# Kernel optimization log

Measured on AMD Instinct MI355X. Metric: run time of the kernel, lower is better.

The kernel has to match this reference:

```python
import jax, jax.numpy as jnp
import numpy as np

DIM = 1024
NUM_HEADS = 16
NUM_KV_HEADS = 4
HEAD_DIM = DIM // NUM_HEADS
ROPE_BASE = 10000.0
EPS = 1e-8
BSZ, SEQ = 8, 1024


def setup_inputs() -> dict:
    key = jax.random.key(0)
    ks = jax.random.split(key, 6)
    x = jax.random.normal(ks[0], (BSZ, SEQ, DIM), dtype=jnp.float32)
    Wq = jax.random.normal(ks[1], (DIM, DIM), dtype=jnp.float32) * 0.02
    Wk = jax.random.normal(ks[2], (NUM_KV_HEADS * HEAD_DIM, DIM), dtype=jnp.float32) * 0.02
    Wv = jax.random.normal(ks[3], (NUM_KV_HEADS * HEAD_DIM, DIM), dtype=jnp.float32) * 0.02
    Wp = jax.random.normal(ks[4], (DIM, DIM), dtype=jnp.float32) * 0.02
    q_gain = jnp.ones((NUM_HEADS,), dtype=jnp.float32)  # qk_gain_init = 1.0
    return {"x": x, "Wq": Wq, "Wk": Wk, "Wv": Wv, "Wp": Wp, "q_gain": q_gain}


def bitlinear(x, w, eps=EPS):
    # weight ternarization (no-grad scale) with STE
    alpha = jax.lax.stop_gradient(jnp.maximum(jnp.mean(jnp.abs(w)), eps))
    w_t = jnp.round(jnp.clip(w / alpha, -1.0, 1.0))
    w_q = w + jax.lax.stop_gradient(w_t * alpha - w)
    # per-token int8 activation fake-quant with STE
    gamma = jax.lax.stop_gradient(
        jnp.maximum(jnp.max(jnp.abs(x), axis=-1, keepdims=True), eps) / 127.0)
    x_int = jnp.round(jnp.clip(x / gamma, -128.0, 127.0))
    x_q = x + jax.lax.stop_gradient(x_int * gamma - x)
    return (x_q @ (w_q / alpha).T) * alpha


def rms_norm(x):
    eps = jnp.finfo(x.dtype).eps
    return x * jax.lax.rsqrt(jnp.mean(x * x, axis=-1, keepdims=True) + eps)


def rope_cache(seq_len, head_dim, base):
    inv_freq = 1.0 / base ** (jnp.arange(0, head_dim, 2, dtype=jnp.float32) / head_dim)
    t = jnp.arange(seq_len, dtype=jnp.float32)
    freqs = jnp.outer(t, inv_freq)  # [S, hd/2]
    return jnp.cos(freqs), jnp.sin(freqs)


def apply_rotary(x, cos, sin):
    # x: [B,H,S,D]; cos/sin: [S,D/2] broadcast over B,H
    half = x.shape[-1] // 2
    x1, x2 = x[..., :half], x[..., half:]
    return jnp.concatenate((x1 * cos + x2 * sin, -x1 * sin + x2 * cos), axis=-1)


def reference(x, Wq, Wk, Wv, Wp, q_gain):
    bsz, seqlen, dim = x.shape
    q = bitlinear(x, Wq).reshape(bsz, seqlen, NUM_HEADS, HEAD_DIM).transpose(0, 2, 1, 3)
    k = bitlinear(x, Wk).reshape(bsz, seqlen, NUM_KV_HEADS, HEAD_DIM).transpose(0, 2, 1, 3)
    v = bitlinear(x, Wv).reshape(bsz, seqlen, NUM_KV_HEADS, HEAD_DIM).transpose(0, 2, 1, 3)
    q = rms_norm(q)
    k = rms_norm(k)
    cos, sin = rope_cache(seqlen, HEAD_DIM, ROPE_BASE)
    q = apply_rotary(q, cos, sin)
    k = apply_rotary(k, cos, sin)
    q = q * q_gain[None, :, None, None]
    # GQA: repeat kv heads
    rep = NUM_HEADS // NUM_KV_HEADS
    k = jnp.repeat(k, rep, axis=1)
    v = jnp.repeat(v, rep, axis=1)
    scale = 1.0 / jnp.sqrt(jnp.float32(HEAD_DIM))
    scores = jnp.einsum('bhqd,bhkd->bhqk', q, k) * scale
    causal = jnp.tril(jnp.ones((seqlen, seqlen), dtype=bool))
    scores = jnp.where(causal, scores, jnp.finfo(scores.dtype).min)
    attn = jax.nn.softmax(scores, axis=-1)
    y = jnp.einsum('bhqk,bhkd->bhqd', attn, v)
    y = y.transpose(0, 2, 1, 3).reshape(bsz, seqlen, dim)
    return bitlinear(y, Wp)
```

## Files before the change

### kernel.cpp

```cpp
#include <hip/hip_runtime.h>
#include <cmath>

#define DIMM 1024
#define NHEADS 16
#define NKV 4
#define HD 64
#define SEQ 1024
#define BSZ 8
#define ROWS (BSZ * SEQ)

typedef unsigned short u16;
typedef signed char s8;
typedef __attribute__((ext_vector_type(8))) short bf16x8;
typedef __attribute__((ext_vector_type(4))) float f32x4;
typedef __attribute__((ext_vector_type(4))) int i32x4;
typedef __attribute__((ext_vector_type(4))) unsigned short u16x4;

static __device__ __forceinline__ u16 f2bf(float f) {
    union { float f; unsigned u; } v; v.f = f;
    unsigned r = v.u + 0x7FFFu + ((v.u >> 16) & 1u);
    return (u16)(r >> 16);
}
static __device__ __forceinline__ float bf2f(u16 h) {
    union { unsigned u; float f; } v; v.u = ((unsigned)h) << 16;
    return v.f;
}

static __device__ __forceinline__ void gload16(const void* g, void* l) {
    __builtin_amdgcn_global_load_lds(
        (const __attribute__((address_space(1))) unsigned int*)g,
        (__attribute__((address_space(3))) unsigned int*)l, 16, 0, 0);
}

__global__ __launch_bounds__(256) void k_absmean_all(const float* __restrict__ Wq,
                                                     const float* __restrict__ Wk,
                                                     const float* __restrict__ Wv,
                                                     const float* __restrict__ Wp,
                                                     float* __restrict__ partial) {
    int wi = blockIdx.x >> 6, local = blockIdx.x & 63;
    const float* w = (wi == 0) ? Wq : (wi == 1) ? Wk : (wi == 2) ? Wv : Wp;
    int n = (wi == 0 || wi == 3) ? 1048576 : 262144;
    float s = 0.f;
    for (int i = local * 256 + threadIdx.x; i < n; i += 64 * 256) s += fabsf(w[i]);
    #pragma unroll
    for (int off = 32; off; off >>= 1) s += __shfl_xor(s, off);
    __shared__ float red[4];
    if ((threadIdx.x & 63) == 0) red[threadIdx.x >> 6] = s;
    __syncthreads();
    if (threadIdx.x == 0) partial[blockIdx.x] = red[0] + red[1] + red[2] + red[3];
}

__global__ __launch_bounds__(256) void k_rope_alpha(float* __restrict__ c, float* __restrict__ s,
                                                    const float* __restrict__ partial,
                                                    float* __restrict__ alpha) {
    int idx = blockIdx.x * 256 + threadIdx.x;
    int t = idx >> 5, i = idx & 31;
    float inv = 1.0f / powf(10000.0f, (float)(2 * i) * (1.0f / 64.0f));
    float f = (float)t * inv;
    c[idx] = cosf(f);
    s[idx] = sinf(f);
    if (blockIdx.x == 0 && threadIdx.x < 4) {
        const int ns[4] = {1048576, 262144, 262144, 1048576};
        float su = 0.f;
        for (int j = 0; j < 64; ++j) su += partial[threadIdx.x * 64 + j];
        alpha[threadIdx.x] = fmaxf(su / (float)ns[threadIdx.x], 1e-8f);
    }
}

__global__ __launch_bounds__(256) void k_tern_all(const float* __restrict__ Wq,
                                                  const float* __restrict__ Wk,
                                                  const float* __restrict__ Wv,
                                                  const float* __restrict__ Wp,
                                                  const float* __restrict__ alpha,
                                                  s8* __restrict__ wtqkv,
                                                  s8* __restrict__ wtp) {
    int idx = blockIdx.x * 256 + threadIdx.x;
    const float* src; s8* dst; float a;
    if (idx < 262144)      { src = Wq + (size_t)idx * 4;            dst = wtqkv + (size_t)idx * 4;                 a = alpha[0]; }
    else if (idx < 327680) { src = Wk + (size_t)(idx - 262144) * 4; dst = wtqkv + 1048576 + (size_t)(idx - 262144) * 4; a = alpha[1]; }
    else if (idx < 393216) { src = Wv + (size_t)(idx - 327680) * 4; dst = wtqkv + 1310720 + (size_t)(idx - 327680) * 4; a = alpha[2]; }
    else                   { src = Wp + (size_t)(idx - 393216) * 4; dst = wtp + (size_t)(idx - 393216) * 4;        a = alpha[3]; }
    float4 v = *reinterpret_cast<const float4*>(src);
    int q0 = (int)rintf(fminf(fmaxf(v.x / a, -1.f), 1.f));
    int q1 = (int)rintf(fminf(fmaxf(v.y / a, -1.f), 1.f));
    int q2 = (int)rintf(fminf(fmaxf(v.z / a, -1.f), 1.f));
    int q3 = (int)rintf(fminf(fmaxf(v.w / a, -1.f), 1.f));
    *reinterpret_cast<unsigned*>(dst) =
        (q0 & 0xff) | ((q1 & 0xff) << 8) | ((q2 & 0xff) << 16) | ((q3 & 0xff) << 24);
}

__global__ __launch_bounds__(256) void k_quant(const float* __restrict__ X,
                                               s8* __restrict__ Xq, float* __restrict__ g) {
    int row = blockIdx.x;
    const float* xr = X + (size_t)row * DIMM;
    float4 v = *reinterpret_cast<const float4*>(&xr[threadIdx.x * 4]);
    float mv = fmaxf(fmaxf(fabsf(v.x), fabsf(v.y)), fmaxf(fabsf(v.z), fabsf(v.w)));
    #pragma unroll
    for (int off = 32; off; off >>= 1) mv = fmaxf(mv, __shfl_xor(mv, off));
    __shared__ float red[4];
    if ((threadIdx.x & 63) == 0) red[threadIdx.x >> 6] = mv;
    __syncthreads();
    mv = fmaxf(fmaxf(red[0], red[1]), fmaxf(red[2], red[3]));
    float gamma = fmaxf(mv, 1e-8f) / 127.0f;
    int q0 = (int)rintf(fminf(fmaxf(v.x / gamma, -128.f), 127.f));
    int q1 = (int)rintf(fminf(fmaxf(v.y / gamma, -128.f), 127.f));
    int q2 = (int)rintf(fminf(fmaxf(v.z / gamma, -128.f), 127.f));
    int q3 = (int)rintf(fminf(fmaxf(v.w / gamma, -128.f), 127.f));
    reinterpret_cast<unsigned*>(Xq + (size_t)row * DIMM)[threadIdx.x] =
        (q0 & 0xff) | ((q1 & 0xff) << 8) | ((q2 & 0xff) << 16) | ((q3 & 0xff) << 24);
    if (threadIdx.x == 0) g[row] = gamma;
}

__global__ __launch_bounds__(256) void k_quant_bf16(const u16* __restrict__ X,
                                                    s8* __restrict__ Xq, float* __restrict__ g) {
    int row = blockIdx.x;
    const u16* xr = X + (size_t)row * DIMM;
    u16x4 h = *reinterpret_cast<const u16x4*>(&xr[threadIdx.x * 4]);
    float v0 = bf2f(h.x), v1 = bf2f(h.y), v2 = bf2f(h.z), v3 = bf2f(h.w);
    float mv = fmaxf(fmaxf(fabsf(v0), fabsf(v1)), fmaxf(fabsf(v2), fabsf(v3)));
    #pragma unroll
    for (int off = 32; off; off >>= 1) mv = fmaxf(mv, __shfl_xor(mv, off));
    __shared__ float red[4];
    if ((threadIdx.x & 63) == 0) red[threadIdx.x >> 6] = mv;
    __syncthreads();
    mv = fmaxf(fmaxf(red[0], red[1]), fmaxf(red[2], red[3]));
    float gamma = fmaxf(mv, 1e-8f) / 127.0f;
    int q0 = (int)rintf(fminf(fmaxf(v0 / gamma, -128.f), 127.f));
    int q1 = (int)rintf(fminf(fmaxf(v1 / gamma, -128.f), 127.f));
    int q2 = (int)rintf(fminf(fmaxf(v2 / gamma, -128.f), 127.f));
    int q3 = (int)rintf(fminf(fmaxf(v3 / gamma, -128.f), 127.f));
    reinterpret_cast<unsigned*>(Xq + (size_t)row * DIMM)[threadIdx.x] =
        (q0 & 0xff) | ((q1 & 0xff) << 8) | ((q2 & 0xff) << 16) | ((q3 & 0xff) << 24);
    if (threadIdx.x == 0) g[row] = gamma;
}

__global__ __launch_bounds__(256) void k_gemm_qkv(const s8* __restrict__ A,
                                                  const s8* __restrict__ B,
                                                  const float* __restrict__ gamma,
                                                  const float* __restrict__ alpha_p,
                                                  const float* __restrict__ rc,
                                                  const float* __restrict__ rs,
                                                  const float* __restrict__ gain,
                                                  u16* __restrict__ Qo,
                                                  u16* __restrict__ Ko,
                                                  float* __restrict__ Cv) {
    __shared__ s8 As[128 * 128];
    __shared__ s8 Bs[128 * 128];
    const int K = DIMM;
    int tid = threadIdx.x;
    int w = tid >> 6, lane = tid & 63;
    int lr = lane & 15, lg = lane >> 4;
    int lr7 = lr & 7;
    int wm = w >> 1, wn = w & 1;
    int row0 = blockIdx.y * 128, col0 = blockIdx.x * 128;

    i32x4 acc[4][4];
    #pragma unroll
    for (int mf = 0; mf < 4; ++mf)
        #pragma unroll
        for (int nf = 0; nf < 4; ++nf) acc[mf][nf] = (i32x4){0, 0, 0, 0};

    int srow = w * 32 + (lane >> 3);
    int scol = 16 * ((lane & 7) ^ (lane >> 3));
    const s8* Ag = A + (size_t)(row0 + srow) * K + scol;
    const s8* Bg = B + (size_t)(col0 + srow) * K + scol;

    for (int k0 = 0; k0 < K; k0 += 128) {
        #pragma unroll
        for (int i = 0; i < 4; ++i) {
            gload16(Ag + (size_t)i * 8 * K + k0, &As[w * 4096 + i * 1024]);
            gload16(Bg + (size_t)i * 8 * K + k0, &Bs[w * 4096 + i * 1024]);
        }
        __syncthreads();
        #pragma unroll
        for (int kh = 0; kh < 2; ++kh) {
            i32x4 af[4], bfr[4];
            #pragma unroll
            for (int mf = 0; mf < 4; ++mf)
                af[mf] = *reinterpret_cast<const i32x4*>(
                    &As[(wm * 64 + mf * 16 + lr) * 128 + 16 * (((kh << 2) + lg) ^ lr7)]);
            #pragma unroll
            for (int nf = 0; nf < 4; ++nf)
                bfr[nf] = *reinterpret_cast<const i32x4*>(
                    &Bs[(wn * 64 + nf * 16 + lr) * 128 + 16 * (((kh << 2) + lg) ^ lr7)]);
            #pragma unroll
            for (int mf = 0; mf < 4; ++mf)
                #pragma unroll
                for (int nf = 0; nf < 4; ++nf)
                    acc[mf][nf] = __builtin_amdgcn_mfma_i32_16x16x64_i8(af[mf], bfr[nf], acc[mf][nf], 0, 0, 0);
        }
        __syncthreads();
    }

    int c0 = col0 + wn * 64;
    int hh = c0 >> 6;
    float alpha = alpha_p[hh < 16 ? 0 : (hh < 20 ? 1 : 2)];
    float ga = (hh < 16) ? gain[hh] * (0.125f * 1.4426950408889634f) : 1.0f;

    #pragma unroll
    for (int mf = 0; mf < 4; ++mf) {
        #pragma unroll
        for (int reg = 0; reg < 4; ++reg) {
            int row = row0 + wm * 64 + mf * 16 + lg * 4 + reg;
            float sc = gamma[row] * alpha;
            float v0 = (float)acc[mf][0][reg] * sc;
            float v1 = (float)acc[mf][1][reg] * sc;
            float v2 = (float)acc[mf][2][reg] * sc;
            float v3 = (float)acc[mf][3][reg] * sc;
            int s = row & 1023, b = row >> 10;
            if (hh < 20) {
                float ss = v0 * v0 + v1 * v1 + v2 * v2 + v3 * v3;
                #pragma unroll
                for (int off = 8; off; off >>= 1) ss += __shfl_xor(ss, off);
                float rn = 1.0f / sqrtf(ss * (1.0f / 64.0f) + 1.1920929e-07f);
                v0 *= rn; v1 *= rn; v2 *= rn; v3 *= rn;
                float cA = rc[s * 32 + lr],      sA = rs[s * 32 + lr];
                float cB = rc[s * 32 + 16 + lr], sB = rs[s * 32 + 16 + lr];
                float y0 = v0 * cA + v2 * sA, y2 = v2 * cA - v0 * sA;
                float y1 = v1 * cB + v3 * sB, y3 = v3 * cB - v1 * sB;
                u16* dst;
                if (hh < 16) {
                    y0 *= ga; y1 *= ga; y2 *= ga; y3 *= ga;
                    dst = Qo + ((size_t)((b * 16 + hh) * 1024 + s)) * 64;
                } else {
                    dst = Ko + ((size_t)((b * 4 + (hh - 16)) * 1024 + s)) * 64;
                }
                dst[lr] = f2bf(y0); dst[16 + lr] = f2bf(y1);
                dst[32 + lr] = f2bf(y2); dst[48 + lr] = f2bf(y3);
            } else {
                float* dst = Cv + (size_t)row * 256 + (hh - 20) * 64;
                dst[lr] = v0; dst[16 + lr] = v1; dst[32 + lr] = v2; dst[48 + lr] = v3;
            }
        }
    }
}

__global__ __launch_bounds__(256) void k_gemm_out(const s8* __restrict__ A,
                                                  const s8* __restrict__ B,
                                                  const float* __restrict__ gamma,
                                                  const float* __restrict__ alpha_p,
                                                  float* __restrict__ C) {
    __shared__ s8 As[128 * 128];
    __shared__ s8 Bs[128 * 128];
    const int K = DIMM;
    int tid = threadIdx.x;
    int w = tid >> 6, lane = tid & 63;
    int lr = lane & 15, lg = lane >> 4;
    int lr7 = lr & 7;
    int wm = w >> 1, wn = w & 1;
    int row0 = blockIdx.y * 128, col0 = blockIdx.x * 128;

    i32x4 acc[4][4];
    #pragma unroll
    for (int mf = 0; mf < 4; ++mf)
        #pragma unroll
        for (int nf = 0; nf < 4; ++nf) acc[mf][nf] = (i32x4){0, 0, 0, 0};

    int srow = w * 32 + (lane >> 3);
    int scol = 16 * ((lane & 7) ^ (lane >> 3));
    const s8* Ag = A + (size_t)(row0 + srow) * K + scol;
    const s8* Bg = B + (size_t)(col0 + srow) * K + scol;

    for (int k0 = 0; k0 < K; k0 += 128) {
        #pragma unroll
        for (int i = 0; i < 4; ++i) {
            gload16(Ag + (size_t)i * 8 * K + k0, &As[w * 4096 + i * 1024]);
            gload16(Bg + (size_t)i * 8 * K + k0, &Bs[w * 4096 + i * 1024]);
        }
        __syncthreads();
        #pragma unroll
        for (int kh = 0; kh < 2; ++kh) {
            i32x4 af[4], bfr[4];
            #pragma unroll
            for (int mf = 0; mf < 4; ++mf)
                af[mf] = *reinterpret_cast<const i32x4*>(
                    &As[(wm * 64 + mf * 16 + lr) * 128 + 16 * (((kh << 2) + lg) ^ lr7)]);
            #pragma unroll
            for (int nf = 0; nf < 4; ++nf)
                bfr[nf] = *reinterpret_cast<const i32x4*>(
                    &Bs[(wn * 64 + nf * 16 + lr) * 128 + 16 * (((kh << 2) + lg) ^ lr7)]);
            #pragma unroll
            for (int mf = 0; mf < 4; ++mf)
                #pragma unroll
                for (int nf = 0; nf < 4; ++nf)
                    acc[mf][nf] = __builtin_amdgcn_mfma_i32_16x16x64_i8(af[mf], bfr[nf], acc[mf][nf], 0, 0, 0);
        }
        __syncthreads();
    }

    float alpha = alpha_p[3];
    #pragma unroll
    for (int mf = 0; mf < 4; ++mf) {
        #pragma unroll
        for (int reg = 0; reg < 4; ++reg) {
            int row = row0 + wm * 64 + mf * 16 + lg * 4 + reg;
            float sc = gamma[row] * alpha;
            #pragma unroll
            for (int nf = 0; nf < 4; ++nf)
                C[(size_t)row * 1024 + col0 + wn * 64 + nf * 16 + lr] = (float)acc[mf][nf][reg] * sc;
        }
    }
}

__global__ __launch_bounds__(256) void k_vtransT(const float* __restrict__ Cv,
                                                 u16* __restrict__ Vt) {
    __shared__ u16 T[64][72];
    int st = blockIdx.x, kv = blockIdx.y, b = blockIdx.z;
    int tid = threadIdx.x;
    int sr = tid >> 4, d4 = tid & 15;
    #pragma unroll
    for (int i = 0; i < 4; ++i) {
        int s = sr + 16 * i;
        int pos = 2 * sr + (i & 1) + 32 * (i >> 1);
        float4 v = *reinterpret_cast<const float4*>(
            &Cv[(size_t)(b * 1024 + st * 64 + s) * 256 + kv * 64 + d4 * 4]);
        T[d4 * 4 + 0][pos] = f2bf(v.x);
        T[d4 * 4 + 1][pos] = f2bf(v.y);
        T[d4 * 4 + 2][pos] = f2bf(v.z);
        T[d4 * 4 + 3][pos] = f2bf(v.w);
    }
    __syncthreads();
    int d = tid >> 2, c = tid & 3;
    float4 o0 = *reinterpret_cast<const float4*>(&T[d][c * 16]);
    float4 o1 = *reinterpret_cast<const float4*>(&T[d][c * 16 + 8]);
    u16* out = &Vt[(((size_t)(b * 4 + kv) * 64) + d) * 1024 + st * 64 + c * 16];
    *reinterpret_cast<float4*>(out) = o0;
    *reinterpret_cast<float4*>(out + 8) = o1;
}

__global__ __launch_bounds__(256) void k_attn_mfma(const u16* __restrict__ Q,
                                                   const u16* __restrict__ K,
                                                   const u16* __restrict__ Vt,
                                                   u16* __restrict__ Y) {
    __shared__ __align__(16) u16 KVs[2][2][4096];
    __shared__ __align__(16) u16 Ps[4][1024];
    int qta = blockIdx.x, qtb = 15 - qta;
    int h = blockIdx.y, b = blockIdx.z;
    int kvh = h >> 2;
    int tid = threadIdx.x;
    int w = tid >> 6, lane = tid & 63;
    int lr = lane & 15, lg = lane >> 4;
    int lr7 = lr & 7;
    int q0a = qta * 64 + w * 16, q0b = qtb * 64 + w * 16;
    const u16* Qb = Q + (((size_t)b * 16 + h) * 1024) * 64;
    const u16* Kb = K + (((size_t)b * 4 + kvh) * 1024) * 64;
    const u16* Vb = Vt + (((size_t)b * 4 + kvh) * 64) * 1024;
    u16* Psw = Ps[w];
    unsigned* Pw32 = reinterpret_cast<unsigned*>(Psw);

    bf16x8 qa0 = *reinterpret_cast<const bf16x8*>(&Qb[(size_t)(q0a + lr) * 64 + 8 * lg]);
    bf16x8 qa1 = *reinterpret_cast<const bf16x8*>(&Qb[(size_t)(q0a + lr) * 64 + 32 + 8 * lg]);
    bf16x8 qb0 = *reinterpret_cast<const bf16x8*>(&Qb[(size_t)(q0b + lr) * 64 + 8 * lg]);
    bf16x8 qb1 = *reinterpret_cast<const bf16x8*>(&Qb[(size_t)(q0b + lr) * 64 + 32 + 8 * lg]);

    float mA[4], lpA[4], mB[4], lpB[4];
    f32x4 accA[4], accB[4];
    #pragma unroll
    for (int r = 0; r < 4; ++r) { mA[r] = -INFINITY; lpA[r] = 0.f; mB[r] = -INFINITY; lpB[r] = 0.f; }
    #pragma unroll
    for (int dt = 0; dt < 4; ++dt) { accA[dt] = (f32x4){0.f,0.f,0.f,0.f}; accB[dt] = (f32x4){0.f,0.f,0.f,0.f}; }

    int sub = lane >> 3, s7 = lane & 7;
    int scol16 = s7 ^ sub;
    int c0 = 2 * w, c1 = 2 * w + 1;

    #define STAGE(buf, t_) do { \
        int kk0 = (t_) * 64; \
        gload16(Kb + (size_t)(kk0 + 8 * c0 + sub) * 64 + scol16 * 8, &KVs[buf][0][c0 * 512]); \
        gload16(Kb + (size_t)(kk0 + 8 * c1 + sub) * 64 + scol16 * 8, &KVs[buf][0][c1 * 512]); \
        gload16(Vb + (size_t)(8 * c0 + sub) * 1024 + kk0 + scol16 * 8, &KVs[buf][1][c0 * 512]); \
        gload16(Vb + (size_t)(8 * c1 + sub) * 1024 + kk0 + scol16 * 8, &KVs[buf][1][c1 * 512]); \
    } while (0)

    STAGE(0, 0);
    asm volatile("s_waitcnt vmcnt(0)" ::: "memory");
    __syncthreads();
    int cur = 0;

    for (int t = 0; t <= qtb; ++t) {
        if (t < qtb) STAGE(cur ^ 1, t + 1);
        const int k0 = t * 64;
        const bool doA = (t <= qta);
        const u16* Kl = KVs[cur][0];
        const u16* Vl = KVs[cur][1];

        float svA[4][4], svB[4][4];
        __builtin_amdgcn_s_setprio(1);
        #pragma unroll
        for (int t4 = 0; t4 < 4; ++t4) {
            int r = t4 * 16 + lr;
            bf16x8 kf0 = *reinterpret_cast<const bf16x8*>(&Kl[r * 64 + ((lg ^ lr7) << 3)]);
            bf16x8 kf1 = *reinterpret_cast<const bf16x8*>(&Kl[r * 64 + (((4 | lg) ^ lr7) << 3)]);
            if (doA) {
                f32x4 z = (f32x4){0.f,0.f,0.f,0.f};
                z = __builtin_amdgcn_mfma_f32_16x16x32_bf16(qa0, kf0, z, 0, 0, 0);
                z = __builtin_amdgcn_mfma_f32_16x16x32_bf16(qa1, kf1, z, 0, 0, 0);
                #pragma unroll
                for (int rr = 0; rr < 4; ++rr) svA[t4][rr] = z[rr];
            }
            f32x4 z2 = (f32x4){0.f,0.f,0.f,0.f};
            z2 = __builtin_amdgcn_mfma_f32_16x16x32_bf16(qb0, kf0, z2, 0, 0, 0);
            z2 = __builtin_amdgcn_mfma_f32_16x16x32_bf16(qb1, kf1, z2, 0, 0, 0);
            #pragma unroll
            for (int rr = 0; rr < 4; ++rr) svB[t4][rr] = z2[rr];
        }
        __builtin_amdgcn_s_setprio(0);
        if (doA && t == qta) {
            #pragma unroll
            for (int t4 = 0; t4 < 4; ++t4) {
                int key = k0 + t4 * 16 + lr;
                #pragma unroll
                for (int rr = 0; rr < 4; ++rr)
                    if (key > q0a + lg * 4 + rr) svA[t4][rr] = -3.0e38f;
            }
        }
        if (t == qtb) {
            #pragma unroll
            for (int t4 = 0; t4 < 4; ++t4) {
                int key = k0 + t4 * 16 + lr;
                #pragma unroll
                for (int rr = 0; rr < 4; ++rr)
                    if (key > q0b + lg * 4 + rr) svB[t4][rr] = -3.0e38f;
            }
        }

        bf16x8 paA0, paA1, paB0, paB1;
        if (doA) {
            float vx[4]; int ok = 1;
            #pragma unroll
            for (int rr = 0; rr < 4; ++rr) {
                vx[rr] = fmaxf(fmaxf(svA[0][rr], svA[1][rr]), fmaxf(svA[2][rr], svA[3][rr]));
                ok &= (vx[rr] <= mA[rr] + 8.0f);
            }
            if (!__all(ok)) {
                #pragma unroll
                for (int rr = 0; rr < 4; ++rr) {
                    float mm = vx[rr];
                    #pragma unroll
                    for (int off = 8; off; off >>= 1) mm = fmaxf(mm, __shfl_xor(mm, off));
                    float mn = fmaxf(mA[rr], mm);
                    float corr = exp2f(mA[rr] - mn);
                    mA[rr] = mn;
                    lpA[rr] *= corr;
                    #pragma unroll
                    for (int dt = 0; dt < 4; ++dt) accA[dt][rr] *= corr;
                }
            }
            #pragma unroll
            for (int rr = 0; rr < 4; ++rr) {
                float p0 = exp2f(svA[0][rr] - mA[rr]);
                float p1 = exp2f(svA[1][rr] - mA[rr]);
                float p2 = exp2f(svA[2][rr] - mA[rr]);
                float p3 = exp2f(svA[3][rr] - mA[rr]);
                lpA[rr] += (p0 + p1) + (p2 + p3);
                unsigned pk01, pk23;
                asm("v_cvt_pk_bf16_f32 %0, %1, %2" : "=v"(pk01) : "v"(p0), "v"(p1));
                asm("v_cvt_pk_bf16_f32 %0, %1, %2" : "=v"(pk23) : "v"(p2), "v"(p3));
                int row = lg * 4 + rr, r7 = row & 7;
                Pw32[row * 32 + (((lr >> 2) ^ r7) << 2) + (lr & 3)] = pk01;
                Pw32[row * 32 + ((((lr >> 2) + 4) ^ r7) << 2) + (lr & 3)] = pk23;
            }
            paA0 = *reinterpret_cast<const bf16x8*>(&Psw[lr * 64 + ((lg ^ lr7) << 3)]);
            paA1 = *reinterpret_cast<const bf16x8*>(&Psw[lr * 64 + (((4 | lg) ^ lr7) << 3)]);
        }

        {
            float vx[4]; int ok = 1;
            #pragma unroll
            for (int rr = 0; rr < 4; ++rr) {
                vx[rr] = fmaxf(fmaxf(svB[0][rr], svB[1][rr]), fmaxf(svB[2][rr], svB[3][rr]));
                ok &= (vx[rr] <= mB[rr] + 8.0f);
            }
            if (!__all(ok)) {
                #pragma unroll
                for (int rr = 0; rr < 4; ++rr) {
                    float mm = vx[rr];
                    #pragma unroll
                    for (int off = 8; off; off >>= 1) mm = fmaxf(mm, __shfl_xor(mm, off));
                    float mn = fmaxf(mB[rr], mm);
                    float corr = exp2f(mB[rr] - mn);
                    mB[rr] = mn;
                    lpB[rr] *= corr;
                    #pragma unroll
                    for (int dt = 0; dt < 4; ++dt) accB[dt][rr] *= corr;
                }
            }
            #pragma unroll
            for (int rr = 0; rr < 4; ++rr) {
                float p0 = exp2f(svB[0][rr] - mB[rr]);
                float p1 = exp2f(svB[1][rr] - mB[rr]);
                float p2 = exp2f(svB[2][rr] - mB[rr]);
                float p3 = exp2f(svB[3][rr] - mB[rr]);
                lpB[rr] += (p0 + p1) + (p2 + p3);
                unsigned pk01, pk23;
                asm("v_cvt_pk_bf16_f32 %0, %1, %2" : "=v"(pk01) : "v"(p0), "v"(p1));
                asm("v_cvt_pk_bf16_f32 %0, %1, %2" : "=v"(pk23) : "v"(p2), "v"(p3));
                int row = lg * 4 + rr, r7 = row & 7;
                Pw32[row * 32 + (((lr >> 2) ^ r7) << 2) + (lr & 3)] = pk01;
                Pw32[row * 32 + ((((lr >> 2) + 4) ^ r7) << 2) + (lr & 3)] = pk23;
            }
            paB0 = *reinterpret_cast<const bf16x8*>(&Psw[lr * 64 + ((lg ^ lr7) << 3)]);
            paB1 = *reinterpret_cast<const bf16x8*>(&Psw[lr * 64 + (((4 | lg) ^ lr7) << 3)]);
        }

        __builtin_amdgcn_s_setprio(1);
        #pragma unroll
        for (int dt = 0; dt < 4; ++dt) {
            int r = dt * 16 + lr;
            bf16x8 vf0 = *reinterpret_cast<const bf16x8*>(&Vl[r * 64 + ((lg ^ lr7) << 3)]);
            bf16x8 vf1 = *reinterpret_cast<const bf16x8*>(&Vl[r * 64 + (((4 | lg) ^ lr7) << 3)]);
            if (doA) {
                accA[dt] = __builtin_amdgcn_mfma_f32_16x16x32_bf16(paA0, vf0, accA[dt], 0, 0, 0);
                accA[dt] = __builtin_amdgcn_mfma_f32_16x16x32_bf16(paA1, vf1, accA[dt], 0, 0, 0);
            }
            accB[dt] = __builtin_amdgcn_mfma_f32_16x16x32_bf16(paB0, vf0, accB[dt], 0, 0, 0);
            accB[dt] = __builtin_amdgcn_mfma_f32_16x16x32_bf16(paB1, vf1, accB[dt], 0, 0, 0);
        }
        __builtin_amdgcn_s_setprio(0);

        asm volatile("s_waitcnt vmcnt(0)" ::: "memory");
        __syncthreads();
        cur ^= 1;
    }
    #undef STAGE

    #pragma unroll
    for (int rr = 0; rr < 4; ++rr) {
        #pragma unroll
        for (int off = 8; off; off >>= 1) {
            lpA[rr] += __shfl_xor(lpA[rr], off);
            lpB[rr] += __shfl_xor(lpB[rr], off);
        }
    }

    #pragma unroll
    for (int rr = 0; rr < 4; ++rr) {
        float invA = 1.0f / lpA[rr];
        float invB = 1.0f / lpB[rr];
        size_t baseA = ((size_t)(b * 1024 + q0a + lg * 4 + rr)) * 1024 + h * 64;
        size_t baseB = ((size_t)(b * 1024 + q0b + lg * 4 + rr)) * 1024 + h * 64;
        #pragma unroll
        for (int dt = 0; dt < 4; ++dt) {
            Y[baseA + dt * 16 + lr] = f2bf(accA[dt][rr] * invA);
            Y[baseB + dt * 16 + lr] = f2bf(accB[dt][rr] * invB);
        }
    }
}

extern "C" void kernel_launch(void* const* d_in, const int* in_sizes, int n_in,
                              void* d_out, int out_size, void* d_ws, size_t ws_size,
                              hipStream_t stream) {
    (void)in_sizes; (void)n_in; (void)out_size; (void)ws_size;
    const float* x  = (const float*)d_in[0];
    const float* Wq = (const float*)d_in[1];
    const float* Wk = (const float*)d_in[2];
    const float* Wv = (const float*)d_in[3];
    const float* Wp = (const float*)d_in[4];
    const float* qg = (const float*)d_in[5];
    float* out = (float*)d_out;

    float* p = (float*)d_ws;
    float* partial = p; p += 256;
    float* alpha = p;   p += 16;
    s8* wtqkv = (s8*)p; p += 393216;
    s8* wtp   = (s8*)p; p += 262144;
    s8* xq    = (s8*)p; p += 2097152;
    float* gam = p; p += 8192;
    u16* y16   = (u16*)p; p += 4194304;
    float* cv  = p; p += 2097152;
    u16* qo = (u16*)p; p += 4194304;
    u16* ko = (u16*)p; p += 1048576;
    u16* vt = (u16*)p; p += 1048576;
    float* rc = p; p += 32768;
    float* rs = p; p += 32768;
    s8* yq = xq;

    k_absmean_all<<<256, 256, 0, stream>>>(Wq, Wk, Wv, Wp, partial);
    k_rope_alpha<<<128, 256, 0, stream>>>(rc, rs, partial, alpha);
    k_tern_all<<<2560, 256, 0, stream>>>(Wq, Wk, Wv, Wp, alpha, wtqkv, wtp);

    k_quant<<<ROWS, 256, 0, stream>>>(x, xq, gam);
    k_gemm_qkv<<<dim3(12, 64), 256, 0, stream>>>(xq, wtqkv, gam, alpha, rc, rs, qg, qo, ko, cv);

    k_vtransT<<<dim3(16, 4, 8), 256, 0, stream>>>(cv, vt);

    k_attn_mfma<<<dim3(8, 16, 8), 256, 0, stream>>>(qo, ko, vt, y16);

    k_quant_bf16<<<ROWS, 256, 0, stream>>>(y16, yq, gam);
    k_gemm_out<<<dim3(8, 64), 256, 0, stream>>>(yq, wtp, gam, alpha, out);
}
```

Baseline: 165.6 us.

## Fuse V transpose into QKV GEMM epilogue and remap workgroups for XCD locality

The QKV GEMM epilogue now converts V tiles to bf16, transposes them through shared memory, and writes Vt directly. This removes the separate k_vtransT kernel and the fp32 Cv intermediate buffer. In addition, the GEMM and attention kernels remap block IDs so that consecutive workgroups on the same XCD (orig&7 grouping) handle neighbouring tiles, aiming for better L2 reuse. The costs are extra shared-memory traffic in the V epilogue and reliance on the block ID distribution pattern.

```diff
diff --git a/kernel.cpp b/kernel.cpp
--- a/kernel.cpp
+++ b/kernel.cpp
@@ -12,6 +12,7 @@
 typedef unsigned short u16;
 typedef signed char s8;
 typedef __attribute__((ext_vector_type(8))) short bf16x8;
+typedef __attribute__((ext_vector_type(8))) unsigned short u16x8;
 typedef __attribute__((ext_vector_type(4))) float f32x4;
 typedef __attribute__((ext_vector_type(4))) int i32x4;
 typedef __attribute__((ext_vector_type(4))) unsigned short u16x4;
@@ -143,16 +144,20 @@
                                                   const float* __restrict__ gain,
                                                   u16* __restrict__ Qo,
                                                   u16* __restrict__ Ko,
-                                                  float* __restrict__ Cv) {
-    __shared__ s8 As[128 * 128];
-    __shared__ s8 Bs[128 * 128];
+                                                  u16* __restrict__ Vt) {
+    __shared__ __align__(16) s8 SMEM[32768];
+    s8* As = SMEM;
+    s8* Bs = SMEM + 16384;
     const int K = DIMM;
     int tid = threadIdx.x;
     int w = tid >> 6, lane = tid & 63;
     int lr = lane & 15, lg = lane >> 4;
     int lr7 = lr & 7;
     int wm = w >> 1, wn = w & 1;
-    int row0 = blockIdx.y * 128, col0 = blockIdx.x * 128;
+    int orig = blockIdx.x + 12 * blockIdx.y;
+    int wgid = (orig & 7) * 96 + (orig >> 3);
+    int bx = wgid % 12, by = wgid / 12;
+    int row0 = by * 128, col0 = bx * 128;
 
     i32x4 acc[4][4];
     #pragma unroll
@@ -195,20 +200,20 @@
     int c0 = col0 + wn * 64;
     int hh = c0 >> 6;
     float alpha = alpha_p[hh < 16 ? 0 : (hh < 20 ? 1 : 2)];
-    float ga = (hh < 16) ? gain[hh] * (0.125f * 1.4426950408889634f) : 1.0f;
-
-    #pragma unroll
-    for (int mf = 0; mf < 4; ++mf) {
-        #pragma unroll
-        for (int reg = 0; reg < 4; ++reg) {
-            int row = row0 + wm * 64 + mf * 16 + lg * 4 + reg;
-            float sc = gamma[row] * alpha;
-            float v0 = (float)acc[mf][0][reg] * sc;
-            float v1 = (float)acc[mf][1][reg] * sc;
-            float v2 = (float)acc[mf][2][reg] * sc;
-            float v3 = (float)acc[mf][3][reg] * sc;
-            int s = row & 1023, b = row >> 10;
-            if (hh < 20) {
+
+    if (hh < 20) {
+        float ga = (hh < 16) ? gain[hh] * (0.125f * 1.4426950408889634f) : 1.0f;
+        #pragma unroll
+        for (int mf = 0; mf < 4; ++mf) {
+            #pragma unroll
+            for (int reg = 0; reg < 4; ++reg) {
+                int row = row0 + wm * 64 + mf * 16 + lg * 4 + reg;
+                float sc = gamma[row] * alpha;
+                float v0 = (float)acc[mf][0][reg] * sc;
+                float v1 = (float)acc[mf][1][reg] * sc;
+                float v2 = (float)acc[mf][2][reg] * sc;
+                float v3 = (float)acc[mf][3][reg] * sc;
+                int s = row & 1023, b = row >> 10;
                 float ss = v0 * v0 + v1 * v1 + v2 * v2 + v3 * v3;
                 #pragma unroll
                 for (int off = 8; off; off >>= 1) ss += __shfl_xor(ss, off);
@@ -227,10 +232,34 @@
                 }
                 dst[lr] = f2bf(y0); dst[16 + lr] = f2bf(y1);
                 dst[32 + lr] = f2bf(y2); dst[48 + lr] = f2bf(y3);
-            } else {
-                float* dst = Cv + (size_t)row * 256 + (hh - 20) * 64;
-                dst[lr] = v0; dst[16 + lr] = v1; dst[32 + lr] = v2; dst[48 + lr] = v3;
-            }
+            }
+        }
+    } else {
+        int kv = hh - 20;
+        u16* T = reinterpret_cast<u16*>(SMEM) + w * 4096;
+        #pragma unroll
+        for (int mf = 0; mf < 4; ++mf) {
+            int pb = (mf & 1) + 32 * (mf >> 1);
+            #pragma unroll
+            for (int reg = 0; reg < 4; ++reg) {
+                int row = row0 + wm * 64 + mf * 16 + lg * 4 + reg;
+                float sc = gamma[row] * alpha;
+                int pos = 2 * (lg * 4 + reg) + pb;
+                #pragma unroll
+                for (int nf = 0; nf < 4; ++nf) {
+                    int d = nf * 16 + lr;
+                    T[d * 64 + (pos ^ (lr7 << 3))] = f2bf((float)acc[mf][nf][reg] * sc);
+                }
+            }
+        }
+        int b = row0 >> 10;
+        int st = ((row0 & 1023) + wm * 64) >> 6;
+        int d = lane, h3 = lane & 7;
+        u16* dst = Vt + (((size_t)(b * 4 + kv) * 64) + d) * 1024 + st * 64;
+        #pragma unroll
+        for (int j = 0; j < 8; ++j) {
+            u16x8 gv = *reinterpret_cast<const u16x8*>(&T[d * 64 + 8 * (j ^ h3)]);
+            *reinterpret_cast<u16x8*>(&dst[8 * j]) = gv;
         }
     }
 }
@@ -248,7 +277,9 @@
     int lr = lane & 15, lg = lane >> 4;
     int lr7 = lr & 7;
     int wm = w >> 1, wn = w & 1;
-    int row0 = blockIdx.y * 128, col0 = blockIdx.x * 128;
+    int orig = blockIdx.x + 8 * blockIdx.y;
+    int wgid = ((orig & 7) << 6) + (orig >> 3);
+    int row0 = (wgid >> 3) * 128, col0 = (wgid & 7) * 128;
 
     i32x4 acc[4][4];
     #pragma unroll
@@ -300,32 +331,6 @@
                 C[(size_t)row * 1024 + col0 + wn * 64 + nf * 16 + lr] = (float)acc[mf][nf][reg] * sc;
         }
     }
-}
-
-__global__ __launch_bounds__(256) void k_vtransT(const float* __restrict__ Cv,
-                                                 u16* __restrict__ Vt) {
-    __shared__ u16 T[64][72];
-    int st = blockIdx.x, kv = blockIdx.y, b = blockIdx.z;
-    int tid = threadIdx.x;
-    int sr = tid >> 4, d4 = tid & 15;
-    #pragma unroll
-    for (int i = 0; i < 4; ++i) {
-        int s = sr + 16 * i;
-        int pos = 2 * sr + (i & 1) + 32 * (i >> 1);
-        float4 v = *reinterpret_cast<const float4*>(
-            &Cv[(size_t)(b * 1024 + st * 64 + s) * 256 + kv * 64 + d4 * 4]);
-        T[d4 * 4 + 0][pos] = f2bf(v.x);
-        T[d4 * 4 + 1][pos] = f2bf(v.y);
-        T[d4 * 4 + 2][pos] = f2bf(v.z);
-        T[d4 * 4 + 3][pos] = f2bf(v.w);
-    }
-    __syncthreads();
-    int d = tid >> 2, c = tid & 3;
-    float4 o0 = *reinterpret_cast<const float4*>(&T[d][c * 16]);
-    float4 o1 = *reinterpret_cast<const float4*>(&T[d][c * 16 + 8]);
-    u16* out = &Vt[(((size_t)(b * 4 + kv) * 64) + d) * 1024 + st * 64 + c * 16];
-    *reinterpret_cast<float4*>(out) = o0;
-    *reinterpret_cast<float4*>(out + 8) = o1;
 }
 
 __global__ __launch_bounds__(256) void k_attn_mfma(const u16* __restrict__ Q,
@@ -334,8 +339,10 @@
                                                    u16* __restrict__ Y) {
     __shared__ __align__(16) u16 KVs[2][2][4096];
     __shared__ __align__(16) u16 Ps[4][1024];
-    int qta = blockIdx.x, qtb = 15 - qta;
-    int h = blockIdx.y, b = blockIdx.z;
+    int orig = blockIdx.x + ((blockIdx.y + (blockIdx.z << 4)) << 3);
+    int wgid = ((orig & 7) << 7) + (orig >> 3);
+    int qta = wgid & 7, qtb = 15 - qta;
+    int h = (wgid >> 3) & 15, b = wgid >> 7;
     int kvh = h >> 2;
     int tid = threadIdx.x;
     int w = tid >> 6, lane = tid & 63;
@@ -567,7 +574,6 @@
     s8* xq    = (s8*)p; p += 2097152;
     float* gam = p; p += 8192;
     u16* y16   = (u16*)p; p += 4194304;
-    float* cv  = p; p += 2097152;
     u16* qo = (u16*)p; p += 4194304;
     u16* ko = (u16*)p; p += 1048576;
     u16* vt = (u16*)p; p += 1048576;
@@ -580,9 +586,7 @@
     k_tern_all<<<2560, 256, 0, stream>>>(Wq, Wk, Wv, Wp, alpha, wtqkv, wtp);
 
     k_quant<<<ROWS, 256, 0, stream>>>(x, xq, gam);
-    k_gemm_qkv<<<dim3(12, 64), 256, 0, stream>>>(xq, wtqkv, gam, alpha, rc, rs, qg, qo, ko, cv);
-
-    k_vtransT<<<dim3(16, 4, 8), 256, 0, stream>>>(cv, vt);
+    k_gemm_qkv<<<dim3(12, 64), 256, 0, stream>>>(xq, wtqkv, gam, alpha, rc, rs, qg, qo, ko, vt);
 
     k_attn_mfma<<<dim3(8, 16, 8), 256, 0, stream>>>(qo, ko, vt, y16);
 
```

New measurement: 156.2 us. 5.6% less time.
